# Kernel optimization log

Hardware: AMD Instinct MI355X
Metric: run time of the kernel (lower is better)

## Reference

```python
import jax, jax.numpy as jnp
import numpy as np

B, IN, HID, OUT, E, C, TOPK = 4096, 1024, 2048, 1024, 8, 1000, 2
EPS = 1e-6


def setup_inputs() -> dict:
    key = jax.random.key(0)
    ks = jax.random.split(key, 8)
    def xavier(k, fan_out, fan_in):
        lim = float(np.sqrt(6.0 / (fan_in + fan_out)))
        return jax.random.uniform(k, (fan_out, fan_in), jnp.float32, -lim, lim)
    return {
        "x": jax.random.normal(ks[0], (B, IN), jnp.float32),
        "Wg": xavier(ks[1], E, IN),
        "bg": jnp.zeros((E,), jnp.float32),
        "gamma": jnp.ones((1, E), jnp.float32),
        "beta": jnp.zeros((1, E), jnp.float32),
        "W1": xavier(ks[2], HID * E, IN),
        "b1": jnp.zeros((HID * E,), jnp.float32),
        "W2": xavier(ks[3], OUT * E, HID * E),
        "b2": jnp.zeros((OUT * E,), jnp.float32),
        "Wc": xavier(ks[4], C, OUT),
        "bc": jnp.zeros((C,), jnp.float32),
    }


def reference(x, Wg, bg, gamma, beta, W1, b1, W2, b2, Wc, bc):
    # gating (noise_std=0 -> no noise)
    gate_logits = x @ Wg.T + bg                      # [B, E]
    # GRN over expert dim
    Gx = jnp.linalg.norm(gate_logits, axis=1, keepdims=True)   # [B, 1]
    Nx = Gx / (jnp.mean(Gx, axis=0, keepdims=True) + EPS)      # [B, 1]
    gate_logits = gamma * (gate_logits * Nx) + beta
    gate_probs = jax.nn.softmax(gate_logits, axis=-1)
    topk_probs, topk_idx = jax.lax.top_k(gate_probs, TOPK)     # [B, K]
    # dense all-expert MLP (fc2 mixes across ALL experts' hidden units, as in source)
    h = jax.nn.relu(x @ W1.T + b1)                   # [B, HID*E]
    eo = (h @ W2.T + b2).reshape(B, E, OUT)          # [B, E, OUT]
    sel = jnp.take_along_axis(eo, topk_idx[:, :, None], axis=1)  # [B, K, OUT]
    out = jnp.einsum('bk,bkd->bd', topk_probs, sel)  # [B, OUT]
    return out @ Wc.T + bc                           # [B, C]
```

## Files before the change

### kernel.cpp

```cpp
#include <hip/hip_runtime.h>
#include <stdint.h>

#define B_SZ   4096
#define IN_SZ  1024
#define NE     8
#define NC     1000
#define HIDE   16384
#define OUTE   1024
#define GEPS   1e-6f
#define NSPLIT 2
#define KSPL   8192

typedef __attribute__((ext_vector_type(8))) short short8;
typedef __attribute__((ext_vector_type(4))) float floatx4;

__device__ __forceinline__ unsigned short f2bf(float f) {
    unsigned u = __float_as_uint(f);
    u += 0x7fffu + ((u >> 16) & 1u);
    return (unsigned short)(u >> 16);
}
__device__ __forceinline__ float bf2f(unsigned short h) {
    return __uint_as_float(((unsigned)h) << 16);
}

__device__ __forceinline__ void async16(const void* g, void* l) {
    __builtin_amdgcn_global_load_lds(
        (const __attribute__((address_space(1))) void*)g,
        (__attribute__((address_space(3))) void*)l, 16, 0, 0);
}

__global__ __launch_bounds__(256) void k_cvt(const float* __restrict__ src,
                                             unsigned short* __restrict__ dst, int n) {
    int i = (blockIdx.x * 256 + threadIdx.x) * 8;
    int stride = gridDim.x * 256 * 8;
    for (; i < n; i += stride) {
        float4 v0 = *(const float4*)(src + i);
        float4 v1 = *(const float4*)(src + i + 4);
        ushort4 o0, o1;
        o0.x = f2bf(v0.x); o0.y = f2bf(v0.y); o0.z = f2bf(v0.z); o0.w = f2bf(v0.w);
        o1.x = f2bf(v1.x); o1.y = f2bf(v1.y); o1.z = f2bf(v1.z); o1.w = f2bf(v1.w);
        uint4 w;
        w.x = (unsigned)o0.x | ((unsigned)o0.y << 16);
        w.y = (unsigned)o0.z | ((unsigned)o0.w << 16);
        w.z = (unsigned)o1.x | ((unsigned)o1.y << 16);
        w.w = (unsigned)o1.z | ((unsigned)o1.w << 16);
        *(uint4*)(dst + i) = w;
    }
}

__global__ __launch_bounds__(256) void k_gate(const float* __restrict__ x,
                                              const float* __restrict__ Wg,
                                              const float* __restrict__ bg,
                                              float* __restrict__ logits,
                                              float* __restrict__ Gx,
                                              unsigned short* __restrict__ xb) {
    int wid = threadIdx.x >> 6, lane = threadIdx.x & 63;
    int b = blockIdx.x * 4 + wid;
    const float* xr = x + (size_t)b * IN_SZ;
    float xv[16];
#pragma unroll
    for (int t = 0; t < 16; ++t) xv[t] = xr[lane + 64 * t];
    unsigned short* xbr = xb + (size_t)b * IN_SZ;
#pragma unroll
    for (int t = 0; t < 16; ++t) xbr[lane + 64 * t] = f2bf(xv[t]);
    float lg[NE];
#pragma unroll
    for (int e = 0; e < NE; ++e) {
        const float* wr = Wg + e * IN_SZ;
        float s = 0.f;
#pragma unroll
        for (int t = 0; t < 16; ++t) s += xv[t] * wr[lane + 64 * t];
#pragma unroll
        for (int m = 32; m >= 1; m >>= 1) s += __shfl_xor(s, m, 64);
        lg[e] = s + bg[e];
    }
    if (lane == 0) {
        float ss = 0.f;
#pragma unroll
        for (int e = 0; e < NE; ++e) { logits[b * NE + e] = lg[e]; ss += lg[e] * lg[e]; }
        Gx[b] = sqrtf(ss);
    }
}

__global__ __launch_bounds__(1024) void k_gsum(const float* __restrict__ Gx,
                                               float* __restrict__ gsum, int* __restrict__ ctrl) {
    __shared__ float sm[1024];
    int t = threadIdx.x;
    if (t < 24) ctrl[t] = 0;
    sm[t] = Gx[t] + Gx[t + 1024] + Gx[t + 2048] + Gx[t + 3072];
    __syncthreads();
    for (int m = 512; m >= 1; m >>= 1) {
        if (t < m) sm[t] += sm[t + m];
        __syncthreads();
    }
    if (t == 0) gsum[0] = sm[0];
}

__global__ __launch_bounds__(256) void k_topk(const float* __restrict__ logits,
                                              const float* __restrict__ Gx,
                                              const float* __restrict__ gsum,
                                              const float* __restrict__ gamma,
                                              const float* __restrict__ beta,
                                              int* __restrict__ tidx, float* __restrict__ tp,
                                              int* __restrict__ counts) {
    int b = blockIdx.x * 256 + threadIdx.x;
    float nx = Gx[b] / (gsum[0] * (1.0f / (float)B_SZ) + GEPS);
    float l[NE];
    float mx = -1e30f;
#pragma unroll
    for (int e = 0; e < NE; ++e) {
        l[e] = gamma[e] * (logits[b * NE + e] * nx) + beta[e];
        mx = fmaxf(mx, l[e]);
    }
    float se = 0.f;
#pragma unroll
    for (int e = 0; e < NE; ++e) { l[e] = expf(l[e] - mx); se += l[e]; }
    float inv = 1.f / se;
    int i0 = 0; float p0 = l[0];
#pragma unroll
    for (int e = 1; e < NE; ++e) if (l[e] > p0) { p0 = l[e]; i0 = e; }
    int i1 = -1; float p1 = -1.f;
#pragma unroll
    for (int e = 0; e < NE; ++e) if (e != i0 && l[e] > p1) { p1 = l[e]; i1 = e; }
    tidx[b * 2 + 0] = i0; tidx[b * 2 + 1] = i1;
    tp[b * 2 + 0] = p0 * inv; tp[b * 2 + 1] = p1 * inv;
    atomicAdd(&counts[i0], 1);
    atomicAdd(&counts[i1], 1);
}

__global__ void k_offsets(const int* __restrict__ counts, int* __restrict__ offs) {
    if (threadIdx.x == 0) {
        int a = 0;
        for (int e = 0; e < NE; ++e) { offs[e] = a; a += counts[e]; }
    }
}

__global__ __launch_bounds__(256) void k_fill(const int* __restrict__ tidx, const float* __restrict__ tp,
                                              const int* __restrict__ offs, int* __restrict__ cursors,
                                              int* __restrict__ rowsw, int* __restrict__ slotof) {
    int b = blockIdx.x * 256 + threadIdx.x;
#pragma unroll
    for (int k = 0; k < 2; ++k) {
        int e = tidx[b * 2 + k];
        int pos = atomicAdd(&cursors[e], 1);
        int at = offs[e] + pos;
        rowsw[at] = b * 2 + k;
        slotof[b * 2 + k] = at;
    }
}


__device__ __forceinline__ void compute_bk64(const short* buf, const int* aoff, const int* boff,
                                             floatx4 acc[4][4]) {
    const short* sA = buf;
    const short* sB = buf + 8192;
    short8 a0[4], a1[4], b0[4], b1[4];
#pragma unroll
    for (int i = 0; i < 4; ++i) {
        a0[i] = *(const short8*)(sA + aoff[i]);
        a1[i] = *(const short8*)(sA + (aoff[i] ^ 32));
        b0[i] = *(const short8*)(sB + boff[i]);
        b1[i] = *(const short8*)(sB + (boff[i] ^ 32));
    }
    asm volatile("s_waitcnt lgkmcnt(0)" ::: "memory");
    __builtin_amdgcn_sched_barrier(0);
    __builtin_amdgcn_s_setprio(1);
#pragma unroll
    for (int i = 0; i < 4; ++i)
#pragma unroll
        for (int j = 0; j < 4; ++j) {
            acc[i][j] = __builtin_amdgcn_mfma_f32_16x16x32_bf16(a0[i], b0[j], acc[i][j], 0, 0, 0);
            acc[i][j] = __builtin_amdgcn_mfma_f32_16x16x32_bf16(a1[i], b1[j], acc[i][j], 0, 0, 0);
        }
    __builtin_amdgcn_s_setprio(0);
}

__device__ __forceinline__ void stage_bk64(const unsigned short* const* pa,
                                           const unsigned short* const* pb,
                                           char* bufc, int koff, int tid) {
#pragma unroll
    for (int c = 0; c < 4; ++c) {
        async16(pa[c] + koff, bufc + c * 4096 + tid * 16);
        async16(pb[c] + koff, bufc + 16384 + c * 4096 + tid * 16);
    }
}

__device__ __forceinline__ void core64db(const unsigned short* const* pa,
                                         const unsigned short* const* pb,
                                         short* smem, int nkt, int wm, int wn,
                                         int tid, int lane, floatx4 acc[4][4]) {
    char* b0c = (char*)smem;
    char* b1c = b0c + 32768;
    const int sl = ((lane >> 4) ^ (lane & 7)) * 8;
    int aoff[4], boff[4];
#pragma unroll
    for (int i = 0; i < 4; ++i) {
        aoff[i] = (wm * 64 + i * 16 + (lane & 15)) * 64 + sl;
        boff[i] = (wn * 64 + i * 16 + (lane & 15)) * 64 + sl;
    }
    stage_bk64(pa, pb, b0c, 0, tid);
    __syncthreads();
#pragma unroll 1
    for (int kt = 0; kt < nkt; kt += 2) {
        if (kt + 1 < nkt) stage_bk64(pa, pb, b1c, (kt + 1) * 64, tid);
        compute_bk64(smem, aoff, boff, acc);
        __syncthreads();
        if (kt + 2 < nkt) stage_bk64(pa, pb, b0c, (kt + 2) * 64, tid);
        compute_bk64(smem + 16384, aoff, boff, acc);
        __syncthreads();
    }
}

__global__ __launch_bounds__(256) void k_h8(const unsigned short* __restrict__ xb,
                                            const unsigned short* __restrict__ w1b,
                                            const float* __restrict__ b1,
                                            unsigned short* __restrict__ hout) {
    extern __shared__ short smem[];
    const int tid = threadIdx.x, lane = tid & 63, wid = tid >> 6;
    const int wm = wid >> 1, wn = wid & 1;
    const int wg = (blockIdx.x & 7) * (gridDim.x >> 3) + (blockIdx.x >> 3);
    const int mt = wg & 31, nt = wg >> 5;
    const int m0 = mt * 128, n0 = nt * 128;
    const int srow = tid >> 3;
    const int cswz = ((tid & 7) ^ (srow & 7)) * 8;
    const unsigned short* pa[4];
    const unsigned short* pb[4];
#pragma unroll
    for (int c = 0; c < 4; ++c) {
        pa[c] = xb  + (size_t)(m0 + 32 * c + srow) * IN_SZ + cswz;
        pb[c] = w1b + (size_t)(n0 + 32 * c + srow) * IN_SZ + cswz;
    }
    floatx4 acc[4][4] = {};
    core64db(pa, pb, smem, IN_SZ / 64, wm, wn, tid, lane, acc);
#pragma unroll
    for (int i = 0; i < 4; ++i)
#pragma unroll
        for (int j = 0; j < 4; ++j)
#pragma unroll
            for (int r = 0; r < 4; ++r) {
                int row = m0 + wm * 64 + i * 16 + (lane >> 4) * 4 + r;
                int col = n0 + wn * 64 + j * 16 + (lane & 15);
                float v = acc[i][j][r] + b1[col];
                hout[(size_t)row * HIDE + col] = f2bf(fmaxf(v, 0.f));
            }
}

__global__ __launch_bounds__(256) void k_moe(const unsigned short* __restrict__ h,
                                             const unsigned short* __restrict__ w2b,
                                             const int* __restrict__ counts,
                                             const int* __restrict__ offs,
                                             const int* __restrict__ rowsw,
                                             unsigned short* __restrict__ parts) {
    const int wg = (blockIdx.x & 7) * (gridDim.x >> 3) + (blockIdx.x >> 3);
    const int mt = wg & 31, nt = (wg >> 5) & 7, sp = (wg >> 8) & 1, e = wg >> 9;
    const int gn = counts[e];
    if (mt * 128 >= gn) return;
    const int gbase = offs[e];
    extern __shared__ short smem[];
    const int tid = threadIdx.x, lane = tid & 63, wid = tid >> 6;
    const int wm = wid >> 1, wn = wid & 1;
    const int srow = tid >> 3;
    const int cswz = ((tid & 7) ^ (srow & 7)) * 8;
    const unsigned short* pa[4];
    const unsigned short* pb[4];
#pragma unroll
    for (int c = 0; c < 4; ++c) {
        int lr = mt * 128 + 32 * c + srow;
        if (lr > gn - 1) lr = gn - 1;
        int grow = rowsw[gbase + lr] >> 1;
        pa[c] = h + (size_t)grow * HIDE + sp * KSPL + cswz;
        pb[c] = w2b + (size_t)(e * OUTE + nt * 128 + 32 * c + srow) * HIDE + sp * KSPL + cswz;
    }
    floatx4 acc[4][4] = {};
    core64db(pa, pb, smem, KSPL / 64, wm, wn, tid, lane, acc);
    unsigned short* pbase = parts + (size_t)sp * B_SZ * 2 * OUTE;
#pragma unroll
    for (int i = 0; i < 4; ++i)
#pragma unroll
        for (int j = 0; j < 4; ++j)
#pragma unroll
            for (int r = 0; r < 4; ++r) {
                int lr = mt * 128 + wm * 64 + i * 16 + (lane >> 4) * 4 + r;
                if (lr < gn) {
                    int at = gbase + lr;
                    int col = nt * 128 + wn * 64 + j * 16 + (lane & 15);
                    pbase[(size_t)at * OUTE + col] = f2bf(acc[i][j][r]);
                }
            }
}

__global__ __launch_bounds__(256) void k_reduce(const unsigned short* __restrict__ parts,
                                                const int* __restrict__ slotof,
                                                const int* __restrict__ tidx,
                                                const float* __restrict__ tp,
                                                const float* __restrict__ b2,
                                                unsigned short* __restrict__ ymix) {
    int i = blockIdx.x * 256 + threadIdx.x;
    int b = i >> 8, col = (i & 255) * 4;
    int at0 = slotof[b * 2], at1 = slotof[b * 2 + 1];
    int e0 = tidx[b * 2], e1 = tidx[b * 2 + 1];
    float q0 = tp[b * 2], q1 = tp[b * 2 + 1];
    float y0[4] = {0.f, 0.f, 0.f, 0.f}, y1[4] = {0.f, 0.f, 0.f, 0.f};
#pragma unroll
    for (int sp = 0; sp < NSPLIT; ++sp) {
        ushort4 u0 = *(const ushort4*)(parts + ((size_t)sp * B_SZ * 2 + at0) * OUTE + col);
        ushort4 u1 = *(const ushort4*)(parts + ((size_t)sp * B_SZ * 2 + at1) * OUTE + col);
        y0[0] += bf2f(u0.x); y0[1] += bf2f(u0.y); y0[2] += bf2f(u0.z); y0[3] += bf2f(u0.w);
        y1[0] += bf2f(u1.x); y1[1] += bf2f(u1.y); y1[2] += bf2f(u1.z); y1[3] += bf2f(u1.w);
    }
    float4 bb0 = *(const float4*)(b2 + (size_t)e0 * OUTE + col);
    float4 bb1 = *(const float4*)(b2 + (size_t)e1 * OUTE + col);
    ushort4 o;
    o.x = f2bf(q0 * (y0[0] + bb0.x) + q1 * (y1[0] + bb1.x));
    o.y = f2bf(q0 * (y0[1] + bb0.y) + q1 * (y1[1] + bb1.y));
    o.z = f2bf(q0 * (y0[2] + bb0.z) + q1 * (y1[2] + bb1.z));
    o.w = f2bf(q0 * (y0[3] + bb0.w) + q1 * (y1[3] + bb1.w));
    *(ushort4*)(ymix + (size_t)b * OUTE + col) = o;
}

__global__ __launch_bounds__(256) void k_gemm_out(const unsigned short* __restrict__ ymix,
                                                  const unsigned short* __restrict__ wcb,
                                                  const float* __restrict__ bc,
                                                  float* __restrict__ out) {
    const int mt = blockIdx.x >> 3, nt = blockIdx.x & 7;
    const int m0 = mt * 128, n0 = nt * 128;
    extern __shared__ short smem[];
    const int tid = threadIdx.x, lane = tid & 63, wid = tid >> 6;
    const int wm = wid >> 1, wn = wid & 1;
    const int srow = tid >> 3;
    const int cswz = ((tid & 7) ^ (srow & 7)) * 8;
    const unsigned short* pa[4];
    const unsigned short* pb[4];
#pragma unroll
    for (int c = 0; c < 4; ++c) {
        pa[c] = ymix + (size_t)(m0 + 32 * c + srow) * IN_SZ + cswz;
        int br = n0 + 32 * c + srow; if (br > NC - 1) br = NC - 1;
        pb[c] = wcb + (size_t)br * IN_SZ + cswz;
    }
    floatx4 acc[4][4] = {};
    core64db(pa, pb, smem, IN_SZ / 64, wm, wn, tid, lane, acc);
#pragma unroll
    for (int i = 0; i < 4; ++i)
#pragma unroll
        for (int j = 0; j < 4; ++j)
#pragma unroll
            for (int r = 0; r < 4; ++r) {
                int row = m0 + wm * 64 + i * 16 + (lane >> 4) * 4 + r;
                int col = n0 + wn * 64 + j * 16 + (lane & 15);
                if (col < NC)
                    out[(size_t)row * NC + col] = acc[i][j][r] + bc[col];
            }
}

extern "C" void kernel_launch(void* const* d_in, const int* in_sizes, int n_in,
                              void* d_out, int out_size, void* d_ws, size_t ws_size,
                              hipStream_t stream) {
    const float* x     = (const float*)d_in[0];
    const float* Wg    = (const float*)d_in[1];
    const float* bg    = (const float*)d_in[2];
    const float* gamma = (const float*)d_in[3];
    const float* beta  = (const float*)d_in[4];
    const float* W1    = (const float*)d_in[5];
    const float* b1    = (const float*)d_in[6];
    const float* W2    = (const float*)d_in[7];
    const float* b2    = (const float*)d_in[8];
    const float* Wc    = (const float*)d_in[9];
    const float* bc    = (const float*)d_in[10];
    float* out = (float*)d_out;

    char* ws = (char*)d_ws;
    size_t o = 0;
    auto carve = [&](size_t bytes) { char* p = ws + o; o += (bytes + 255) & ~(size_t)255; return p; };
    unsigned short* xb    = (unsigned short*)carve((size_t)B_SZ * IN_SZ * 2);
    unsigned short* w1b   = (unsigned short*)carve((size_t)HIDE * IN_SZ * 2);
    unsigned short* w2b   = (unsigned short*)carve((size_t)NE * OUTE * HIDE * 2);
    unsigned short* wcb   = (unsigned short*)carve((size_t)NC * IN_SZ * 2);
    unsigned short* h     = (unsigned short*)carve((size_t)B_SZ * HIDE * 2);
    unsigned short* parts = (unsigned short*)carve((size_t)NSPLIT * B_SZ * 2 * OUTE * 2);
    unsigned short* ymix  = (unsigned short*)carve((size_t)B_SZ * OUTE * 2);
    float* logits = (float*)carve((size_t)B_SZ * NE * 4);
    float* Gx     = (float*)carve((size_t)B_SZ * 4);
    int*   tidx   = (int*)carve((size_t)B_SZ * 2 * 4);
    float* tp     = (float*)carve((size_t)B_SZ * 2 * 4);
    int*   rowsw  = (int*)carve((size_t)B_SZ * 2 * 4);
    int*   slotof = (int*)carve((size_t)B_SZ * 2 * 4);
    int*   ctrl   = (int*)carve(256);
    int* counts  = ctrl;
    int* cursors = ctrl + 8;
    int* offs    = ctrl + 16;
    float* gsum  = (float*)(ctrl + 24);

    hipFuncSetAttribute((const void*)k_h8,       hipFuncAttributeMaxDynamicSharedMemorySize, 65536);
    hipFuncSetAttribute((const void*)k_moe,      hipFuncAttributeMaxDynamicSharedMemorySize, 65536);
    hipFuncSetAttribute((const void*)k_gemm_out, hipFuncAttributeMaxDynamicSharedMemorySize, 65536);

    k_cvt<<<2048, 256, 0, stream>>>(W1, w1b, HIDE * IN_SZ);
    k_cvt<<<2048, 256, 0, stream>>>(W2, w2b, NE * OUTE * HIDE);
    k_cvt<<<512,  256, 0, stream>>>(Wc, wcb, NC * IN_SZ);

    k_gate<<<B_SZ / 4, 256, 0, stream>>>(x, Wg, bg, logits, Gx, xb);
    k_gsum<<<1, 1024, 0, stream>>>(Gx, gsum, ctrl);
    k_topk<<<B_SZ / 256, 256, 0, stream>>>(logits, Gx, gsum, gamma, beta, tidx, tp, counts);
    k_offsets<<<1, 64, 0, stream>>>(counts, offs);
    k_fill<<<B_SZ / 256, 256, 0, stream>>>(tidx, tp, offs, cursors, rowsw, slotof);

    k_h8<<<(B_SZ / 128) * (HIDE / 128), 256, 65536, stream>>>(xb, w1b, b1, h);
    k_moe<<<NE * 32 * 8 * NSPLIT, 256, 65536, stream>>>(h, w2b, counts, offs, rowsw, parts);
    k_reduce<<<B_SZ, 256, 0, stream>>>(parts, slotof, tidx, tp, b2, ymix);
    k_gemm_out<<<(B_SZ / 128) * 8, 256, 65536, stream>>>(ymix, wcb, bc, out);
}
```

Measured before the change: 922.3 us.

## Fuse weight conversions into gate and fc1 kernels to overlap with compute

Removes the three standalone fp32-to-bf16 weight conversion launches. The W1 and Wc conversions now run as extra blocks of the gate kernel, and the W2 conversion (the largest) runs as every fifth block of the fc1 GEMM kernel. The memory-bound conversion can then overlap with the compute-bound GEMM and launch overhead drops. The risk is that conversion blocks contend for bandwidth and CU slots with GEMM tiles, and that the fixed block-index remapping changes tile scheduling order.

```diff
diff --git a/kernel.cpp b/kernel.cpp
--- a/kernel.cpp
+++ b/kernel.cpp
@@ -29,33 +29,41 @@
         (__attribute__((address_space(3))) void*)l, 16, 0, 0);
 }
 
-__global__ __launch_bounds__(256) void k_cvt(const float* __restrict__ src,
-                                             unsigned short* __restrict__ dst, int n) {
-    int i = (blockIdx.x * 256 + threadIdx.x) * 8;
-    int stride = gridDim.x * 256 * 8;
+__device__ __forceinline__ void cvt_span(const float* __restrict__ src,
+                                         unsigned short* __restrict__ dst,
+                                         int n, int bid, int nb) {
+    int i = (bid * 256 + (int)threadIdx.x) * 8;
+    int stride = nb * 256 * 8;
     for (; i < n; i += stride) {
         float4 v0 = *(const float4*)(src + i);
         float4 v1 = *(const float4*)(src + i + 4);
-        ushort4 o0, o1;
-        o0.x = f2bf(v0.x); o0.y = f2bf(v0.y); o0.z = f2bf(v0.z); o0.w = f2bf(v0.w);
-        o1.x = f2bf(v1.x); o1.y = f2bf(v1.y); o1.z = f2bf(v1.z); o1.w = f2bf(v1.w);
         uint4 w;
-        w.x = (unsigned)o0.x | ((unsigned)o0.y << 16);
-        w.y = (unsigned)o0.z | ((unsigned)o0.w << 16);
-        w.z = (unsigned)o1.x | ((unsigned)o1.y << 16);
-        w.w = (unsigned)o1.z | ((unsigned)o1.w << 16);
+        w.x = (unsigned)f2bf(v0.x) | ((unsigned)f2bf(v0.y) << 16);
+        w.y = (unsigned)f2bf(v0.z) | ((unsigned)f2bf(v0.w) << 16);
+        w.z = (unsigned)f2bf(v1.x) | ((unsigned)f2bf(v1.y) << 16);
+        w.w = (unsigned)f2bf(v1.z) | ((unsigned)f2bf(v1.w) << 16);
         *(uint4*)(dst + i) = w;
     }
 }
 
-__global__ __launch_bounds__(256) void k_gate(const float* __restrict__ x,
-                                              const float* __restrict__ Wg,
-                                              const float* __restrict__ bg,
-                                              float* __restrict__ logits,
-                                              float* __restrict__ Gx,
-                                              unsigned short* __restrict__ xb) {
+__global__ __launch_bounds__(256) void k_gatef(const float* __restrict__ x,
+                                               const float* __restrict__ Wg,
+                                               const float* __restrict__ bg,
+                                               float* __restrict__ logits,
+                                               float* __restrict__ Gx,
+                                               unsigned short* __restrict__ xb,
+                                               const float* __restrict__ W1,
+                                               unsigned short* __restrict__ w1b,
+                                               const float* __restrict__ Wc,
+                                               unsigned short* __restrict__ wcb) {
+    const int bid = blockIdx.x;
+    if (bid >= 1024) {
+        if (bid < 1536) cvt_span(W1, w1b, HIDE * IN_SZ, bid - 1024, 512);
+        else            cvt_span(Wc, wcb, NC * IN_SZ,   bid - 1536, 64);
+        return;
+    }
     int wid = threadIdx.x >> 6, lane = threadIdx.x & 63;
-    int b = blockIdx.x * 4 + wid;
+    int b = bid * 4 + wid;
     const float* xr = x + (size_t)b * IN_SZ;
     float xv[16];
 #pragma unroll
@@ -211,14 +219,23 @@
     }
 }
 
-__global__ __launch_bounds__(256) void k_h8(const unsigned short* __restrict__ xb,
-                                            const unsigned short* __restrict__ w1b,
-                                            const float* __restrict__ b1,
-                                            unsigned short* __restrict__ hout) {
+__global__ __launch_bounds__(256) void k_h8f(const unsigned short* __restrict__ xb,
+                                             const unsigned short* __restrict__ w1b,
+                                             const float* __restrict__ b1,
+                                             unsigned short* __restrict__ hout,
+                                             const float* __restrict__ W2,
+                                             unsigned short* __restrict__ w2b) {
+    const int bid = blockIdx.x;
+    const int role = bid % 5;
+    if (role == 4) {
+        cvt_span(W2, w2b, NE * OUTE * HIDE, bid / 5, 1024);
+        return;
+    }
+    const int hbid = (bid / 5) * 4 + role;
     extern __shared__ short smem[];
     const int tid = threadIdx.x, lane = tid & 63, wid = tid >> 6;
     const int wm = wid >> 1, wn = wid & 1;
-    const int wg = (blockIdx.x & 7) * (gridDim.x >> 3) + (blockIdx.x >> 3);
+    const int wg = (hbid & 7) * 512 + (hbid >> 3);
     const int mt = wg & 31, nt = wg >> 5;
     const int m0 = mt * 128, n0 = nt * 128;
     const int srow = tid >> 3;
@@ -390,21 +407,17 @@
     int* offs    = ctrl + 16;
     float* gsum  = (float*)(ctrl + 24);
 
-    hipFuncSetAttribute((const void*)k_h8,       hipFuncAttributeMaxDynamicSharedMemorySize, 65536);
+    hipFuncSetAttribute((const void*)k_h8f,      hipFuncAttributeMaxDynamicSharedMemorySize, 65536);
     hipFuncSetAttribute((const void*)k_moe,      hipFuncAttributeMaxDynamicSharedMemorySize, 65536);
     hipFuncSetAttribute((const void*)k_gemm_out, hipFuncAttributeMaxDynamicSharedMemorySize, 65536);
 
-    k_cvt<<<2048, 256, 0, stream>>>(W1, w1b, HIDE * IN_SZ);
-    k_cvt<<<2048, 256, 0, stream>>>(W2, w2b, NE * OUTE * HIDE);
-    k_cvt<<<512,  256, 0, stream>>>(Wc, wcb, NC * IN_SZ);
-
-    k_gate<<<B_SZ / 4, 256, 0, stream>>>(x, Wg, bg, logits, Gx, xb);
+    k_gatef<<<1600, 256, 0, stream>>>(x, Wg, bg, logits, Gx, xb, W1, w1b, Wc, wcb);
     k_gsum<<<1, 1024, 0, stream>>>(Gx, gsum, ctrl);
     k_topk<<<B_SZ / 256, 256, 0, stream>>>(logits, Gx, gsum, gamma, beta, tidx, tp, counts);
     k_offsets<<<1, 64, 0, stream>>>(counts, offs);
     k_fill<<<B_SZ / 256, 256, 0, stream>>>(tidx, tp, offs, cursors, rowsw, slotof);
 
-    k_h8<<<(B_SZ / 128) * (HIDE / 128), 256, 65536, stream>>>(xb, w1b, b1, h);
+    k_h8f<<<5120, 256, 65536, stream>>>(xb, w1b, b1, h, W2, w2b);
     k_moe<<<NE * 32 * 8 * NSPLIT, 256, 65536, stream>>>(h, w2b, counts, offs, rowsw, parts);
     k_reduce<<<B_SZ, 256, 0, stream>>>(parts, slotof, tidx, tp, b2, ymix);
     k_gemm_out<<<(B_SZ / 128) * 8, 256, 65536, stream>>>(ymix, wcb, bc, out);
```

New measurement: 898.2 us. 2.6% less time.
